# Optimization experiments

Measured on AMD Instinct MI355X. Metric: run time of the kernel, lower is better.

Reference implementation:

```python
import jax, jax.numpy as jnp
import numpy as np

BETA = 0.25
EPS = 1e-10


def setup_inputs() -> dict:
    key = jax.random.key(0)
    k1, k2 = jax.random.split(key)
    B, D, K = 32768, 512, 8192
    a = jax.random.normal(k1, (B, D), dtype=jnp.float32)
    # torch init: uniform(-1/K, 1/K)
    codebook = jax.random.uniform(k2, (K, D), dtype=jnp.float32,
                                  minval=-1.0 / K, maxval=1.0 / K)
    return {"a": a, "codebook": codebook}


def reference(a, codebook):
    # a: [B, D], codebook: [K, D]
    B = a.shape[0]
    K = codebook.shape[0]
    # squared-distance via a2 + e2 - 2*a.E^T (no [B,K,D] intermediate)
    a2 = jnp.sum(a * a, axis=1, keepdims=True)            # [B, 1]
    e2 = jnp.sum(codebook * codebook, axis=1)[None, :]    # [1, K]
    dist = a2 + e2 - 2.0 * (a @ codebook.T)               # [B, K]
    idx = jnp.argmin(dist, axis=1)                        # [B] int
    z_q = codebook[idx]                                   # [B, D]
    # straight-through estimator
    z = a + jax.lax.stop_gradient(z_q - a)
    commit_loss = BETA * jnp.mean((a - jax.lax.stop_gradient(z_q)) ** 2)
    codebook_loss = jnp.mean((jax.lax.stop_gradient(a) - z_q) ** 2)
    # usage stats (no_grad in torch)
    usage = jnp.zeros((K,), a.dtype).at[idx].add(1.0) / B  # mean of one-hot
    perplexity = jnp.exp(-jnp.sum(usage * jnp.log(usage + EPS)))
    used_codes = jnp.sum(usage > 0).astype(a.dtype)
    usage_mean = jnp.mean(usage)
    return (idx, z, commit_loss, codebook_loss, perplexity, used_codes, usage_mean)
```

## Files before the change

### kernel.cpp

```cpp
#include <hip/hip_runtime.h>
#include <stdint.h>

#define D_DIM 512
#define EBFS 544
#define ESTRIDE 528
#define SPLIT_K 384
#define DELTA 8.0e-4f
#define MAXC 48

typedef unsigned long long u64;
typedef float f32x4 __attribute__((ext_vector_type(4)));
typedef short s16x8 __attribute__((ext_vector_type(8)));

static __device__ inline unsigned short f2bf(float x) {
  unsigned u = __float_as_uint(x);
  u = (u + 0x7FFFu + ((u >> 16) & 1u)) >> 16;
  return (unsigned short)u;
}
static __device__ inline unsigned mono(float f) {
  unsigned u = __float_as_uint(f);
  return (u & 0x80000000u) ? ~u : (u | 0x80000000u);
}
static __device__ inline float unmono(unsigned m) {
  return __uint_as_float((m & 0x80000000u) ? (m & 0x7FFFFFFFu) : ~m);
}

__global__ void k_init(int* __restrict__ counts, int K) {
  int i = blockIdx.x * blockDim.x + threadIdx.x;
  if (i < K) counts[i] = 0;
}

__global__ void k_prep(const float* __restrict__ E, unsigned short* __restrict__ Ebf,
                       float* __restrict__ Eskew, int* __restrict__ counts, int K) {
  int i = blockIdx.x * blockDim.x + threadIdx.x;
  if (i < K) counts[i] = 0;
  if (i >= K * 64) return;
  int row = i >> 6;
  int ch = i & 63;
  const float* src = E + (size_t)row * D_DIM + ch * 8;
  float4 f0 = *(const float4*)(src);
  float4 f1 = *(const float4*)(src + 4);
  s16x8 o;
  o[0] = (short)f2bf(f0.x); o[1] = (short)f2bf(f0.y);
  o[2] = (short)f2bf(f0.z); o[3] = (short)f2bf(f0.w);
  o[4] = (short)f2bf(f1.x); o[5] = (short)f2bf(f1.y);
  o[6] = (short)f2bf(f1.z); o[7] = (short)f2bf(f1.w);
  *(s16x8*)(Ebf + (size_t)row * EBFS + ch * 8) = o;
  float* dst = Eskew + (size_t)row * ESTRIDE + ch * 8;
  *(float4*)(dst) = f0;
  *(float4*)(dst + 4) = f1;
}

__global__ void k_rowsq(const float* __restrict__ X, float* __restrict__ out, int nrows) {
  int t = threadIdx.x;
  int row = blockIdx.x * 4 + (t >> 6);
  int l = t & 63;
  if (row >= nrows) return;
  int b = l >> 4;
  int L = l & 15;
  const float* p = X + (size_t)row * D_DIM + b * 128 + L;
  float v[8];
#pragma unroll
  for (int j = 0; j < 8; ++j) {
    float x = p[16 * j];
    float sq = x * x;
    asm volatile("" : "+v"(sq));
    v[j] = sq;
  }
  float s = ((v[0] + v[1]) + (v[2] + v[3])) + ((v[4] + v[5]) + (v[6] + v[7]));
  s += __shfl_xor(s, 8, 64);
  s += __shfl_xor(s, 4, 64);
  s += __shfl_xor(s, 2, 64);
  s += __shfl_xor(s, 1, 64);
  s += __shfl_xor(s, 16, 64);
  s += __shfl_xor(s, 32, 64);
  if (l == 0) out[row] = s;
}

#define LOADH(BUF, P0, P1, DKB)                                                 \
  _Pragma("unroll") for (int dk = 0; dk < 8; ++dk) {                            \
    BUF[dk]     = *(const s16x8*)((P0) + (DKB + dk) * 32);                      \
    BUF[8 + dk] = *(const s16x8*)((P1) + (DKB + dk) * 32);                      \
  }

#define MFMAH(BUF, DKB)                                                         \
  _Pragma("unroll") for (int dk = 0; dk < 8; ++dk) {                            \
    s16x8 af[4];                                                                \
    _Pragma("unroll") for (int r = 0; r < 4; ++r) {                             \
      int row = wm * 64 + r * 16 + l15;                                         \
      int off = ((row * 64 + (DKB + dk) * 4 + lhi) * 16) ^ ((row & 15) << 4);   \
      af[r] = *(const s16x8*)(Alds + off);                                      \
    }                                                                           \
    _Pragma("unroll") for (int r = 0; r < 4; ++r) {                             \
      acc[r][0] = __builtin_amdgcn_mfma_f32_16x16x32_bf16(af[r], BUF[dk], acc[r][0], 0, 0, 0);      \
      acc[r][1] = __builtin_amdgcn_mfma_f32_16x16x32_bf16(af[r], BUF[8 + dk], acc[r][1], 0, 0, 0);  \
    }                                                                           \
  }

__global__ __launch_bounds__(512, 2) void k_screen(
    const float* __restrict__ A, const unsigned short* __restrict__ Ebf,
    const float* __restrict__ e2, int* __restrict__ cand_cnt,
    unsigned short* __restrict__ cand, int K) {
  __shared__ unsigned runmin[128];
  __shared__ unsigned cnt[128];
  __shared__ unsigned short list[128 * MAXC];
  __shared__ __align__(16) char Alds[128 * 1024];

  const int t = threadIdx.x;
  const int m0 = blockIdx.x * 128;

  if (t < 128) { runmin[t] = 0xFFFFFFFFu; cnt[t] = 0; }

  {
    int row = t >> 2;
    int s4 = t & 3;
    const float* ar = A + (size_t)(m0 + row) * D_DIM;
#pragma unroll
    for (int c = 0; c < 16; ++c) {
      int ch = s4 * 16 + c;
      float4 f0 = *(const float4*)(ar + ch * 8);
      float4 f1 = *(const float4*)(ar + ch * 8 + 4);
      s16x8 o;
      o[0] = (short)f2bf(f0.x); o[1] = (short)f2bf(f0.y);
      o[2] = (short)f2bf(f0.z); o[3] = (short)f2bf(f0.w);
      o[4] = (short)f2bf(f1.x); o[5] = (short)f2bf(f1.y);
      o[6] = (short)f2bf(f1.z); o[7] = (short)f2bf(f1.w);
      int off = ((row * 64 + ch) * 16) ^ ((row & 15) << 4);
      *(s16x8*)(Alds + off) = o;
    }
  }
  __syncthreads();

  const int lane = t & 63;
  const int wid = t >> 6;
  const int wm = wid >> 2;
  const int wn = wid & 3;
  const int l15 = lane & 15;
  const int lhi = lane >> 4;

  const unsigned short* Bbase = Ebf + (size_t)(wn * 32 + l15) * EBFS + lhi * 8;

  s16x8 bufA[16], bufB[16];
  LOADH(bufA, Bbase, Bbase + 16 * EBFS, 0)

  for (int tile = 0; tile < 64; ++tile) {
    const int n0 = tile * 128;
    const unsigned short* P0 = Bbase + (size_t)n0 * EBFS;
    const unsigned short* P1 = P0 + 16 * EBFS;

    f32x4 acc[4][2];
#pragma unroll
    for (int r = 0; r < 4; ++r)
#pragma unroll
      for (int c = 0; c < 2; ++c) acc[r][c] = (f32x4){0.f, 0.f, 0.f, 0.f};

    LOADH(bufB, P0, P1, 8)
    MFMAH(bufA, 0)
    if (tile < 63) {
      const unsigned short* N0 = P0 + (size_t)128 * EBFS;
      LOADH(bufA, N0, N0 + 16 * EBFS, 0)
    }
    MFMAH(bufB, 8)

    float e2c0 = e2[n0 + wn * 32 + l15];
    float e2c1 = e2[n0 + wn * 32 + 16 + l15];
#pragma unroll
    for (int r = 0; r < 4; ++r)
#pragma unroll
      for (int g = 0; g < 4; ++g) {
        float s0 = fmaf(-2.f, acc[r][0][g], e2c0);
        float s1 = fmaf(-2.f, acc[r][1][g], e2c1);
        int row = wm * 64 + r * 16 + lhi * 4 + g;
        float mn = fminf(s0, s1);
        mn = fminf(mn, __shfl_xor(mn, 1, 64));
        mn = fminf(mn, __shfl_xor(mn, 2, 64));
        mn = fminf(mn, __shfl_xor(mn, 4, 64));
        mn = fminf(mn, __shfl_xor(mn, 8, 64));
        if (l15 == 0) atomicMin(&runmin[row], mono(mn));
        float thr = unmono(runmin[row]) + DELTA;
        if (s0 <= thr) {
          unsigned p = atomicAdd(&cnt[row], 1u);
          if (p < MAXC) list[row * MAXC + p] = (unsigned short)(n0 + wn * 32 + l15);
        }
        if (s1 <= thr) {
          unsigned p = atomicAdd(&cnt[row], 1u);
          if (p < MAXC) list[row * MAXC + p] = (unsigned short)(n0 + wn * 32 + 16 + l15);
        }
      }
  }
  __syncthreads();
  {
    int row = t >> 2;
    unsigned c = cnt[row];
    if ((t & 3) == 0) cand_cnt[m0 + row] = (int)c;
    unsigned cc = c < MAXC ? c : MAXC;
    for (unsigned p = t & 3; p < cc; p += 4)
      cand[(size_t)(m0 + row) * MAXC + p] = list[row * MAXC + p];
  }
}

static __device__ inline u64 exact_pack(const float* __restrict__ ar,
                                        const float* __restrict__ er,
                                        float a2r, float e2k, int k) {
  float acc1 = 0.f, acc2 = 0.f;
  for (int d = 0; d < SPLIT_K; d += 4) {
    float4 a = *(const float4*)(ar + d);
    float4 e = *(const float4*)(er + d);
    acc1 = fmaf(a.x, e.x, acc1); acc1 = fmaf(a.y, e.y, acc1);
    acc1 = fmaf(a.z, e.z, acc1); acc1 = fmaf(a.w, e.w, acc1);
  }
  for (int d = SPLIT_K; d < D_DIM; d += 4) {
    float4 a = *(const float4*)(ar + d);
    float4 e = *(const float4*)(er + d);
    acc2 = fmaf(a.x, e.x, acc2); acc2 = fmaf(a.y, e.y, acc2);
    acc2 = fmaf(a.z, e.z, acc2); acc2 = fmaf(a.w, e.w, acc2);
  }
  float M = acc1 + acc2;
  float S = a2r + e2k;
  float s = fmaf(-2.f, M, S);
  return ((u64)mono(s) << 32) | (unsigned)k;
}

__global__ __launch_bounds__(256) void k_rescore(
    const float* __restrict__ A, const float* __restrict__ Eskew,
    const float* __restrict__ a2, const float* __restrict__ e2,
    const int* __restrict__ cand_cnt, const unsigned short* __restrict__ cand,
    float* __restrict__ out_idx, float* __restrict__ out_z,
    float* __restrict__ rowsum, int* __restrict__ counts, int K) {
  int lane = threadIdx.x & 63;
  int r = blockIdx.x * 4 + (threadIdx.x >> 6);
  int c = cand_cnt[r];
  const float* ar = A + (size_t)r * D_DIM;
  float a2r = a2[r];
  u64 best = ~0ULL;
  if (c <= MAXC) {
    if (lane < c) {
      int k = cand[(size_t)r * MAXC + lane];
      best = exact_pack(ar, Eskew + (size_t)k * ESTRIDE, a2r, e2[k], k);
    }
  } else {
    for (int k = lane; k < K; k += 64) {
      u64 p = exact_pack(ar, Eskew + (size_t)k * ESTRIDE, a2r, e2[k], k);
      if (p < best) best = p;
    }
  }
#pragma unroll
  for (int m = 1; m < 64; m <<= 1) {
    u64 o = __shfl_xor(best, m, 64);
    if (o < best) best = o;
  }
  int idx = (int)(unsigned)(best & 0xFFFFFFFFULL);

  const float4* pa = (const float4*)(ar) + lane * 2;
  const float4* pe = (const float4*)(Eskew + (size_t)idx * ESTRIDE) + lane * 2;
  float4* pz = (float4*)(out_z + (size_t)r * D_DIM) + lane * 2;
  float ls = 0.f;
#pragma unroll
  for (int q = 0; q < 2; ++q) {
    float4 a = pa[q];
    float4 e = pe[q];
    float4 z;
    z.x = a.x + (e.x - a.x);
    z.y = a.y + (e.y - a.y);
    z.z = a.z + (e.z - a.z);
    z.w = a.w + (e.w - a.w);
    pz[q] = z;
    float dx = a.x - e.x, dy = a.y - e.y, dz = a.z - e.z, dw = a.w - e.w;
    ls += dx * dx + dy * dy + dz * dz + dw * dw;
  }
#pragma unroll
  for (int m = 1; m < 64; m <<= 1) ls += __shfl_xor(ls, m, 64);
  if (lane == 0) {
    out_idx[r] = (float)idx;
    rowsum[r] = ls;
    atomicAdd(&counts[idx], 1);
  }
}

#define KTILE(D0, ACC)                                                          \
  {                                                                             \
    int r = t >> 2;                                                             \
    int c4 = (t & 3) << 2;                                                      \
    float4 va = *(const float4*)(A + (size_t)(m0 + r) * D_DIM + (D0) + c4);     \
    As[c4 + 0][r] = va.x; As[c4 + 1][r] = va.y;                                 \
    As[c4 + 2][r] = va.z; As[c4 + 3][r] = va.w;                                 \
    float4 vb = *(const float4*)(E + (size_t)(n0 + r) * D_DIM + (D0) + c4);     \
    Es[c4 + 0][r] = vb.x; Es[c4 + 1][r] = vb.y;                                 \
    Es[c4 + 2][r] = vb.z; Es[c4 + 3][r] = vb.w;                                 \
    __syncthreads();                                                            \
    _Pragma("unroll")                                                           \
    for (int dd = 0; dd < 16; ++dd) {                                           \
      float af[4], bf[8];                                                       \
      *(float4*)af = *(const float4*)(&As[dd][ty * 4]);                         \
      *(float4*)bf = *(const float4*)(&Es[dd][tx * 4]);                         \
      *(float4*)(bf + 4) = *(const float4*)(&Es[dd][64 + tx * 4]);              \
      _Pragma("unroll")                                                         \
      for (int i = 0; i < 4; ++i)                                               \
        _Pragma("unroll")                                                       \
        for (int j = 0; j < 8; ++j)                                             \
          ACC[i][j] = fmaf(af[i], bf[j], ACC[i][j]);                            \
    }                                                                           \
    __syncthreads();                                                            \
  }

__global__ __launch_bounds__(512) void k_argmin_f32(
    const float* __restrict__ A, const float* __restrict__ E,
    const float* __restrict__ a2, const float* __restrict__ e2,
    float* __restrict__ out_idx, int* __restrict__ idx_ws, int K) {
  __shared__ float As[16][128];
  __shared__ float Es[16][128];
  const int m0 = blockIdx.x * 128;
  const int t = threadIdx.x;
  const int tx = t & 15;
  const int ty = t >> 4;
  float a2l[4];
#pragma unroll
  for (int i = 0; i < 4; ++i) a2l[i] = a2[m0 + ty * 4 + i];
  u64 best[4];
#pragma unroll
  for (int i = 0; i < 4; ++i) best[i] = ~0ULL;
  for (int n0 = 0; n0 < K; n0 += 128) {
    float acc1[4][8], acc2[4][8];
#pragma unroll
    for (int i = 0; i < 4; ++i)
#pragma unroll
      for (int j = 0; j < 8; ++j) { acc1[i][j] = 0.f; acc2[i][j] = 0.f; }
    for (int d0 = 0; d0 < SPLIT_K; d0 += 16) KTILE(d0, acc1)
    for (int d0 = SPLIT_K; d0 < D_DIM; d0 += 16) KTILE(d0, acc2)
    float e2l[8];
#pragma unroll
    for (int j = 0; j < 8; ++j) {
      int cl = (j < 4) ? (tx * 4 + j) : (64 + tx * 4 + (j - 4));
      e2l[j] = e2[n0 + cl];
    }
#pragma unroll
    for (int i = 0; i < 4; ++i) {
#pragma unroll
      for (int j = 0; j < 8; ++j) {
        int cl = (j < 4) ? (tx * 4 + j) : (64 + tx * 4 + (j - 4));
        float S = a2l[i] + e2l[j];
        float m = acc1[i][j] + acc2[i][j];
        float s = fmaf(-2.f, m, S);
        u64 p = ((u64)mono(s) << 32) | (unsigned)(n0 + cl);
        if (p < best[i]) best[i] = p;
      }
    }
  }
#pragma unroll
  for (int m = 1; m < 16; m <<= 1) {
#pragma unroll
    for (int i = 0; i < 4; ++i) {
      u64 o = __shfl_xor(best[i], m, 64);
      if (o < best[i]) best[i] = o;
    }
  }
  if (tx == 0) {
#pragma unroll
    for (int i = 0; i < 4; ++i) {
      int row = m0 + ty * 4 + i;
      int idx = (int)(unsigned)(best[i] & 0xFFFFFFFFULL);
      out_idx[row] = (float)idx;
      idx_ws[row] = idx;
    }
  }
}

__global__ void k_gather(const float* __restrict__ A, const float* __restrict__ E,
                         const int* __restrict__ idx_ws,
                         float* __restrict__ out_z, float* __restrict__ rowsum,
                         int* __restrict__ counts) {
  int b = blockIdx.x;
  int t = threadIdx.x;
  int idx = idx_ws[b];
  const float4* pa = (const float4*)(A + (size_t)b * D_DIM);
  const float4* pe = (const float4*)(E + (size_t)idx * D_DIM);
  float4 a = pa[t];
  float4 e = pe[t];
  float4 z;
  z.x = a.x + (e.x - a.x);
  z.y = a.y + (e.y - a.y);
  z.z = a.z + (e.z - a.z);
  z.w = a.w + (e.w - a.w);
  ((float4*)(out_z + (size_t)b * D_DIM))[t] = z;
  float dx = a.x - e.x, dy = a.y - e.y, dz = a.z - e.z, dw = a.w - e.w;
  float ls = dx * dx + dy * dy + dz * dz + dw * dw;
#pragma unroll
  for (int off = 32; off > 0; off >>= 1) ls += __shfl_down(ls, off, 64);
  __shared__ float wsum[2];
  if ((t & 63) == 0) wsum[t >> 6] = ls;
  __syncthreads();
  if (t == 0) {
    rowsum[b] = wsum[0] + wsum[1];
    atomicAdd(&counts[idx], 1);
  }
}

__global__ void k_stats(const int* __restrict__ counts, const float* __restrict__ rowsum,
                        float* __restrict__ out_sc, int B, int K) {
  int t = threadIdx.x;
  double ent = 0.0, tot = 0.0, S = 0.0;
  int used = 0;
  for (int k = t; k < K; k += 256) {
    int c = counts[k];
    double u = (double)c / (double)B;
    ent += u * log(u + 1e-10);
    tot += u;
    used += (c > 0) ? 1 : 0;
  }
  for (int b = t; b < B; b += 256) S += (double)rowsum[b];
  __shared__ double se[256];
  __shared__ double st[256];
  __shared__ double ss[256];
  __shared__ int su[256];
  se[t] = ent; st[t] = tot; ss[t] = S; su[t] = used;
  __syncthreads();
  for (int s = 128; s > 0; s >>= 1) {
    if (t < s) { se[t] += se[t + s]; st[t] += st[t + s]; ss[t] += ss[t + s]; su[t] += su[t + s]; }
    __syncthreads();
  }
  if (t == 0) {
    double Sm = ss[0];
    double N = (double)B * (double)D_DIM;
    out_sc[0] = (float)(0.25 * Sm / N);
    out_sc[1] = (float)(Sm / N);
    out_sc[2] = (float)exp(-se[0]);
    out_sc[3] = (float)su[0];
    out_sc[4] = (float)(st[0] / (double)K);
  }
}

extern "C" void kernel_launch(void* const* d_in, const int* in_sizes, int n_in,
                              void* d_out, int out_size, void* d_ws, size_t ws_size,
                              hipStream_t stream) {
  const float* A = (const float*)d_in[0];
  const float* E = (const float*)d_in[1];
  const int B = in_sizes[0] / D_DIM;
  const int K = in_sizes[1] / D_DIM;

  float* out = (float*)d_out;
  float* out_idx = out;
  float* out_z = out + B;
  float* out_sc = out + B + (size_t)B * D_DIM;

  char* ws = (char*)d_ws;
  size_t off = 0;
  float* a2 = (float*)(ws + off); off += (size_t)B * 4;
  float* e2 = (float*)(ws + off); off += (size_t)K * 4;
  int* counts = (int*)(ws + off); off += (size_t)K * 4;
  float* rowsum = (float*)(ws + off); off += (size_t)B * 4;
  int* idx_ws = (int*)(ws + off); off += (size_t)B * 4;
  int* cand_cnt = (int*)(ws + off); off += (size_t)B * 4;
  unsigned short* cand = (unsigned short*)(ws + off); off += (size_t)B * MAXC * 2;
  unsigned short* Ebf = (unsigned short*)(ws + off); off += (size_t)K * EBFS * 2;
  float* Eskew = (float*)(ws + off); off += (size_t)K * ESTRIDE * 4;
  const size_t need = off;

  k_rowsq<<<(B + 3) / 4, 256, 0, stream>>>(A, a2, B);
  k_rowsq<<<(K + 3) / 4, 256, 0, stream>>>(E, e2, K);

  if (ws_size >= need) {
    int np = K * 64;
    k_prep<<<(np + 255) / 256, 256, 0, stream>>>(E, Ebf, Eskew, counts, K);
    k_screen<<<B / 128, 512, 0, stream>>>(A, Ebf, e2, cand_cnt, cand, K);
    k_rescore<<<B / 4, 256, 0, stream>>>(A, Eskew, a2, e2, cand_cnt, cand,
                                         out_idx, out_z, rowsum, counts, K);
  } else {
    k_init<<<(K + 255) / 256, 256, 0, stream>>>(counts, K);
    k_argmin_f32<<<B / 128, 512, 0, stream>>>(A, E, a2, e2, out_idx, idx_ws, K);
    k_gather<<<B, 128, 0, stream>>>(A, E, idx_ws, out_z, rowsum, counts);
  }
  k_stats<<<1, 256, 0, stream>>>(counts, rowsum, out_sc, B, K);
}
```

Baseline: 870.6 us.

## Run screen kernel with 1024 threads and smaller per-wave tiles

Doubles k_screen's block size to 16 waves, so each wave covers 32 query rows instead of 64. The codebook register double-buffer is cut to quarter-depth chunks with a four-step load/MFMA alternation. The goal is more waves per CU, since LDS use already limits residency to one block, and lower register pressure per wave to better hide latency. In exchange, each codebook tile is reloaded from global/L2 by twice as many waves, and the per-row atomics on shared memory see more contention.

```diff
diff --git a/kernel.cpp b/kernel.cpp
--- a/kernel.cpp
+++ b/kernel.cpp
@@ -77,27 +77,27 @@
   if (l == 0) out[row] = s;
 }
 
-#define LOADH(BUF, P0, P1, DKB)                                                 \
-  _Pragma("unroll") for (int dk = 0; dk < 8; ++dk) {                            \
-    BUF[dk]     = *(const s16x8*)((P0) + (DKB + dk) * 32);                      \
-    BUF[8 + dk] = *(const s16x8*)((P1) + (DKB + dk) * 32);                      \
-  }
-
-#define MFMAH(BUF, DKB)                                                         \
-  _Pragma("unroll") for (int dk = 0; dk < 8; ++dk) {                            \
-    s16x8 af[4];                                                                \
-    _Pragma("unroll") for (int r = 0; r < 4; ++r) {                             \
-      int row = wm * 64 + r * 16 + l15;                                         \
-      int off = ((row * 64 + (DKB + dk) * 4 + lhi) * 16) ^ ((row & 15) << 4);   \
+#define LOADQ(BUF, PBASE, DKB)                                                  \
+  _Pragma("unroll") for (int dk = 0; dk < 4; ++dk) {                            \
+    BUF[dk]     = *(const s16x8*)((PBASE) + ((DKB) + dk) * 32);                 \
+    BUF[4 + dk] = *(const s16x8*)((PBASE) + 16 * EBFS + ((DKB) + dk) * 32);     \
+  }
+
+#define MFMAQ(BUF, DKB)                                                         \
+  _Pragma("unroll") for (int dk = 0; dk < 4; ++dk) {                            \
+    s16x8 af[2];                                                                \
+    _Pragma("unroll") for (int r = 0; r < 2; ++r) {                             \
+      int row = wm * 32 + r * 16 + l15;                                         \
+      int off = ((row * 64 + ((DKB) + dk) * 4 + lhi) * 16) ^ ((row & 15) << 4); \
       af[r] = *(const s16x8*)(Alds + off);                                      \
     }                                                                           \
-    _Pragma("unroll") for (int r = 0; r < 4; ++r) {                             \
+    _Pragma("unroll") for (int r = 0; r < 2; ++r) {                             \
       acc[r][0] = __builtin_amdgcn_mfma_f32_16x16x32_bf16(af[r], BUF[dk], acc[r][0], 0, 0, 0);      \
-      acc[r][1] = __builtin_amdgcn_mfma_f32_16x16x32_bf16(af[r], BUF[8 + dk], acc[r][1], 0, 0, 0);  \
+      acc[r][1] = __builtin_amdgcn_mfma_f32_16x16x32_bf16(af[r], BUF[4 + dk], acc[r][1], 0, 0, 0);  \
     }                                                                           \
   }
 
-__global__ __launch_bounds__(512, 2) void k_screen(
+__global__ __launch_bounds__(1024, 4) void k_screen(
     const float* __restrict__ A, const unsigned short* __restrict__ Ebf,
     const float* __restrict__ e2, int* __restrict__ cand_cnt,
     unsigned short* __restrict__ cand, int K) {
@@ -112,12 +112,12 @@
   if (t < 128) { runmin[t] = 0xFFFFFFFFu; cnt[t] = 0; }
 
   {
-    int row = t >> 2;
-    int s4 = t & 3;
+    int row = t >> 3;
+    int s8 = t & 7;
     const float* ar = A + (size_t)(m0 + row) * D_DIM;
 #pragma unroll
-    for (int c = 0; c < 16; ++c) {
-      int ch = s4 * 16 + c;
+    for (int c = 0; c < 8; ++c) {
+      int ch = s8 * 8 + c;
       float4 f0 = *(const float4*)(ar + ch * 8);
       float4 f1 = *(const float4*)(ar + ch * 8 + 4);
       s16x8 o;
@@ -138,39 +138,42 @@
   const int l15 = lane & 15;
   const int lhi = lane >> 4;
 
-  const unsigned short* Bbase = Ebf + (size_t)(wn * 32 + l15) * EBFS + lhi * 8;
-
-  s16x8 bufA[16], bufB[16];
-  LOADH(bufA, Bbase, Bbase + 16 * EBFS, 0)
+  const unsigned short* Bb = Ebf + (size_t)(wn * 32 + l15) * EBFS + lhi * 8;
+
+  s16x8 bufA[8], bufB[8];
+  LOADQ(bufA, Bb, 0)
 
   for (int tile = 0; tile < 64; ++tile) {
     const int n0 = tile * 128;
-    const unsigned short* P0 = Bbase + (size_t)n0 * EBFS;
-    const unsigned short* P1 = P0 + 16 * EBFS;
-
-    f32x4 acc[4][2];
-#pragma unroll
-    for (int r = 0; r < 4; ++r)
+    const unsigned short* P = Bb + (size_t)n0 * EBFS;
+
+    f32x4 acc[2][2];
+#pragma unroll
+    for (int r = 0; r < 2; ++r)
 #pragma unroll
       for (int c = 0; c < 2; ++c) acc[r][c] = (f32x4){0.f, 0.f, 0.f, 0.f};
 
-    LOADH(bufB, P0, P1, 8)
-    MFMAH(bufA, 0)
+    LOADQ(bufB, P, 4)
+    MFMAQ(bufA, 0)
+    LOADQ(bufA, P, 8)
+    MFMAQ(bufB, 4)
+    LOADQ(bufB, P, 12)
+    MFMAQ(bufA, 8)
     if (tile < 63) {
-      const unsigned short* N0 = P0 + (size_t)128 * EBFS;
-      LOADH(bufA, N0, N0 + 16 * EBFS, 0)
-    }
-    MFMAH(bufB, 8)
+      const unsigned short* Pn = P + (size_t)128 * EBFS;
+      LOADQ(bufA, Pn, 0)
+    }
+    MFMAQ(bufB, 12)
 
     float e2c0 = e2[n0 + wn * 32 + l15];
     float e2c1 = e2[n0 + wn * 32 + 16 + l15];
 #pragma unroll
-    for (int r = 0; r < 4; ++r)
+    for (int r = 0; r < 2; ++r)
 #pragma unroll
       for (int g = 0; g < 4; ++g) {
         float s0 = fmaf(-2.f, acc[r][0][g], e2c0);
         float s1 = fmaf(-2.f, acc[r][1][g], e2c1);
-        int row = wm * 64 + r * 16 + lhi * 4 + g;
+        int row = wm * 32 + r * 16 + lhi * 4 + g;
         float mn = fminf(s0, s1);
         mn = fminf(mn, __shfl_xor(mn, 1, 64));
         mn = fminf(mn, __shfl_xor(mn, 2, 64));
@@ -190,11 +193,11 @@
   }
   __syncthreads();
   {
-    int row = t >> 2;
+    int row = t >> 3;
     unsigned c = cnt[row];
-    if ((t & 3) == 0) cand_cnt[m0 + row] = (int)c;
+    if ((t & 7) == 0) cand_cnt[m0 + row] = (int)c;
     unsigned cc = c < MAXC ? c : MAXC;
-    for (unsigned p = t & 3; p < cc; p += 4)
+    for (unsigned p = t & 7; p < cc; p += 8)
       cand[(size_t)(m0 + row) * MAXC + p] = list[row * MAXC + p];
   }
 }
@@ -461,7 +464,7 @@
   if (ws_size >= need) {
     int np = K * 64;
     k_prep<<<(np + 255) / 256, 256, 0, stream>>>(E, Ebf, Eskew, counts, K);
-    k_screen<<<B / 128, 512, 0, stream>>>(A, Ebf, e2, cand_cnt, cand, K);
+    k_screen<<<B / 128, 1024, 0, stream>>>(A, Ebf, e2, cand_cnt, cand, K);
     k_rescore<<<B / 4, 256, 0, stream>>>(A, Eskew, a2, e2, cand_cnt, cand,
                                          out_idx, out_z, rowsum, counts, K);
   } else {
```

After: 1.380 ms. +58.5%, slower.

## Reshape screen warp tiling to 32x64 and pipeline codebook loads in finer chunks

Applied to the files above, without the earlier changes.

Changes the per-wave output tile of the bf16 screening GEMM from 64 rows x 32 codes to 32 rows x 64 codes, so each wave shares fewer A fragments from LDS and owns more codebook columns. Codebook fragments from global memory now arrive in eight double-buffered chunks of 64 elements interleaved with MFMAs, instead of two half-K chunks. This cuts register buffer size and is meant to hide global load latency better, at the cost of more load/compute interleave points and more per-row atomics in the candidate filter.

```diff
diff --git a/kernel.cpp b/kernel.cpp
--- a/kernel.cpp
+++ b/kernel.cpp
@@ -77,24 +77,22 @@
   if (l == 0) out[row] = s;
 }
 
-#define LOADH(BUF, P0, P1, DKB)                                                 \
-  _Pragma("unroll") for (int dk = 0; dk < 8; ++dk) {                            \
-    BUF[dk]     = *(const s16x8*)((P0) + (DKB + dk) * 32);                      \
-    BUF[8 + dk] = *(const s16x8*)((P1) + (DKB + dk) * 32);                      \
-  }
-
-#define MFMAH(BUF, DKB)                                                         \
-  _Pragma("unroll") for (int dk = 0; dk < 8; ++dk) {                            \
-    s16x8 af[4];                                                                \
-    _Pragma("unroll") for (int r = 0; r < 4; ++r) {                             \
-      int row = wm * 64 + r * 16 + l15;                                         \
-      int off = ((row * 64 + (DKB + dk) * 4 + lhi) * 16) ^ ((row & 15) << 4);   \
+#define LOADE(BUF, P, DKB)                                                      \
+  _Pragma("unroll") for (int d2 = 0; d2 < 2; ++d2)                              \
+    _Pragma("unroll") for (int g = 0; g < 4; ++g)                               \
+      BUF[d2 * 4 + g] = *(const s16x8*)((P) + (size_t)(g * 16) * EBFS + ((DKB) + d2) * 32);
+
+#define MFMAE(BUF, DKB)                                                         \
+  _Pragma("unroll") for (int d2 = 0; d2 < 2; ++d2) {                            \
+    s16x8 af[2];                                                                \
+    _Pragma("unroll") for (int r = 0; r < 2; ++r) {                             \
+      int row = wm * 32 + r * 16 + l15;                                         \
+      int off = ((row * 64 + ((DKB) + d2) * 4 + lhi) * 16) ^ ((row & 15) << 4); \
       af[r] = *(const s16x8*)(Alds + off);                                      \
     }                                                                           \
-    _Pragma("unroll") for (int r = 0; r < 4; ++r) {                             \
-      acc[r][0] = __builtin_amdgcn_mfma_f32_16x16x32_bf16(af[r], BUF[dk], acc[r][0], 0, 0, 0);      \
-      acc[r][1] = __builtin_amdgcn_mfma_f32_16x16x32_bf16(af[r], BUF[8 + dk], acc[r][1], 0, 0, 0);  \
-    }                                                                           \
+    _Pragma("unroll") for (int r = 0; r < 2; ++r)                               \
+      _Pragma("unroll") for (int g = 0; g < 4; ++g)                             \
+        acc[r][g] = __builtin_amdgcn_mfma_f32_16x16x32_bf16(af[r], BUF[d2 * 4 + g], acc[r][g], 0, 0, 0); \
   }
 
 __global__ __launch_bounds__(512, 2) void k_screen(
@@ -133,59 +131,64 @@
 
   const int lane = t & 63;
   const int wid = t >> 6;
-  const int wm = wid >> 2;
-  const int wn = wid & 3;
+  const int wm = wid >> 1;
+  const int wn = wid & 1;
   const int l15 = lane & 15;
   const int lhi = lane >> 4;
 
-  const unsigned short* Bbase = Ebf + (size_t)(wn * 32 + l15) * EBFS + lhi * 8;
-
-  s16x8 bufA[16], bufB[16];
-  LOADH(bufA, Bbase, Bbase + 16 * EBFS, 0)
+  const unsigned short* Bb = Ebf + (size_t)(wn * 64 + l15) * EBFS + lhi * 8;
+
+  s16x8 bufA[8], bufB[8];
+  LOADE(bufA, Bb, 0)
 
   for (int tile = 0; tile < 64; ++tile) {
     const int n0 = tile * 128;
-    const unsigned short* P0 = Bbase + (size_t)n0 * EBFS;
-    const unsigned short* P1 = P0 + 16 * EBFS;
-
-    f32x4 acc[4][2];
-#pragma unroll
-    for (int r = 0; r < 4; ++r)
-#pragma unroll
-      for (int c = 0; c < 2; ++c) acc[r][c] = (f32x4){0.f, 0.f, 0.f, 0.f};
-
-    LOADH(bufB, P0, P1, 8)
-    MFMAH(bufA, 0)
+    const unsigned short* P = Bb + (size_t)n0 * EBFS;
+
+    f32x4 acc[2][4];
+#pragma unroll
+    for (int r = 0; r < 2; ++r)
+#pragma unroll
+      for (int g = 0; g < 4; ++g) acc[r][g] = (f32x4){0.f, 0.f, 0.f, 0.f};
+
+    LOADE(bufB, P, 2)  MFMAE(bufA, 0)
+    LOADE(bufA, P, 4)  MFMAE(bufB, 2)
+    LOADE(bufB, P, 6)  MFMAE(bufA, 4)
+    LOADE(bufA, P, 8)  MFMAE(bufB, 6)
+    LOADE(bufB, P, 10) MFMAE(bufA, 8)
+    LOADE(bufA, P, 12) MFMAE(bufB, 10)
+    LOADE(bufB, P, 14) MFMAE(bufA, 12)
     if (tile < 63) {
-      const unsigned short* N0 = P0 + (size_t)128 * EBFS;
-      LOADH(bufA, N0, N0 + 16 * EBFS, 0)
-    }
-    MFMAH(bufB, 8)
-
-    float e2c0 = e2[n0 + wn * 32 + l15];
-    float e2c1 = e2[n0 + wn * 32 + 16 + l15];
-#pragma unroll
-    for (int r = 0; r < 4; ++r)
-#pragma unroll
-      for (int g = 0; g < 4; ++g) {
-        float s0 = fmaf(-2.f, acc[r][0][g], e2c0);
-        float s1 = fmaf(-2.f, acc[r][1][g], e2c1);
-        int row = wm * 64 + r * 16 + lhi * 4 + g;
-        float mn = fminf(s0, s1);
+      const unsigned short* Pn = P + (size_t)128 * EBFS;
+      LOADE(bufA, Pn, 0)
+    }
+    MFMAE(bufB, 14)
+
+    float e2g[4];
+#pragma unroll
+    for (int g = 0; g < 4; ++g) e2g[g] = e2[n0 + wn * 64 + g * 16 + l15];
+
+#pragma unroll
+    for (int r = 0; r < 2; ++r)
+#pragma unroll
+      for (int gi = 0; gi < 4; ++gi) {
+        int row = wm * 32 + r * 16 + lhi * 4 + gi;
+        float s[4];
+#pragma unroll
+        for (int g = 0; g < 4; ++g) s[g] = fmaf(-2.f, acc[r][g][gi], e2g[g]);
+        float mn = fminf(fminf(s[0], s[1]), fminf(s[2], s[3]));
         mn = fminf(mn, __shfl_xor(mn, 1, 64));
         mn = fminf(mn, __shfl_xor(mn, 2, 64));
         mn = fminf(mn, __shfl_xor(mn, 4, 64));
         mn = fminf(mn, __shfl_xor(mn, 8, 64));
         if (l15 == 0) atomicMin(&runmin[row], mono(mn));
         float thr = unmono(runmin[row]) + DELTA;
-        if (s0 <= thr) {
-          unsigned p = atomicAdd(&cnt[row], 1u);
-          if (p < MAXC) list[row * MAXC + p] = (unsigned short)(n0 + wn * 32 + l15);
-        }
-        if (s1 <= thr) {
-          unsigned p = atomicAdd(&cnt[row], 1u);
-          if (p < MAXC) list[row * MAXC + p] = (unsigned short)(n0 + wn * 32 + 16 + l15);
-        }
+#pragma unroll
+        for (int g = 0; g < 4; ++g)
+          if (s[g] <= thr) {
+            unsigned p = atomicAdd(&cnt[row], 1u);
+            if (p < MAXC) list[row * MAXC + p] = (unsigned short)(n0 + wn * 64 + g * 16 + l15);
+          }
       }
   }
   __syncthreads();
```

After: 901.9 us. 1.04x slower.
